# Kernel tuning notes

Hardware: AMD Instinct MI355X
Metric: run time of the kernel (lower is better)

## Reference

```python
import jax, jax.numpy as jnp
import numpy as np


def setup_inputs() -> dict:
    key = jax.random.key(0)
    k1, k2 = jax.random.split(key)
    B, C, H, W = 16, 32, 256, 256
    OH, OW = 256, 256
    Im = jax.random.normal(k1, (B, C, H, W), dtype=jnp.float32)
    # pixel-space sampling coordinates in [0, W-1] / [0, H-1]
    gx = jax.random.uniform(k2, (B, 1, OH, OW), dtype=jnp.float32) * (W - 1)
    gy = jax.random.uniform(jax.random.fold_in(k2, 1), (B, 1, OH, OW), dtype=jnp.float32) * (H - 1)
    G = jnp.concatenate([gx, gy], axis=1)  # [B, 2, OH, OW]
    return {"Im": Im, "G": G}


def reference(Im, G):
    # replicate-pad by 1 on each spatial side
    Imp = jnp.pad(Im, ((0, 0), (0, 0), (1, 1), (1, 1)), mode='edge')
    B, C, H, W = Imp.shape
    _, _, OH, OW = G.shape
    # flatten coords per batch; +1 accounts for the pad
    x = G[:, 0].reshape(B, -1) + 1.0  # [B, OH*OW]
    y = G[:, 1].reshape(B, -1) + 1.0
    max_x, max_y = W - 1, H - 1
    x0 = jnp.floor(x).astype(jnp.int32)
    y0 = jnp.floor(y).astype(jnp.int32)
    x1 = x0 + 1
    y1 = y0 + 1
    x0 = jnp.clip(x0, 0, max_x)
    x1 = jnp.clip(x1, 0, max_x)
    y0 = jnp.clip(y0, 0, max_y)
    y1 = jnp.clip(y1, 0, max_y)
    # [B, H*W, C] channels-last flat image, gather per batch
    Im_flat = Imp.transpose(0, 2, 3, 1).reshape(B, H * W, C)

    def gather(yi, xi):
        idx = yi * W + xi  # [B, OH*OW]
        return jnp.take_along_axis(Im_flat, idx[:, :, None], axis=1)  # [B, OH*OW, C]

    Ia = gather(y0, x0)
    Ib = gather(y1, x0)
    Ic = gather(y0, x1)
    Id = gather(y1, x1)
    dx = x1.astype(jnp.float32) - x  # note: uses clamped x1, as in the original
    dy = y1.astype(jnp.float32) - y
    wa = (dy * dx)[:, :, None]
    wb = ((1.0 - dy) * dx)[:, :, None]
    wc = (dy * (1.0 - dx))[:, :, None]
    wd = ((1.0 - dy) * (1.0 - dx))[:, :, None]
    out = wa * Ia + wb * Ib + wc * Ic + wd * Id  # [B, OH*OW, C]
    return out.reshape(B, OH, OW, C).transpose(0, 3, 1, 2)
```

## Files before the change

### kernel.cpp

```cpp
#include <hip/hip_runtime.h>

#define BB 16
#define CC 32
#define HH 256
#define WW 256
#define OHH 256
#define OWW 256
#define HW  (HH * WW)

typedef _Float16 half8 __attribute__((ext_vector_type(8)));
typedef _Float16 half4v __attribute__((ext_vector_type(4)));
typedef float float4v __attribute__((ext_vector_type(4)));

__global__ __launch_bounds__(256) void nchw_to_nhwc_h(
    const float* __restrict__ Im,
    _Float16* __restrict__ dst)
{
    __shared__ float lds[64 * 33];
    int blk  = blockIdx.x;
    int xcd  = blk & 7;
    int slot = blk >> 3;
    int b    = xcd + 8 * (slot >> 10);
    int inner = slot & 1023;
    int h  = inner >> 2;
    int w0 = (inner & 3) * 64;
    int t  = threadIdx.x;

    const float* src = Im + ((size_t)b * CC * HH + h) * WW;

    #pragma unroll
    for (int i = 0; i < 2; ++i) {
        int idx = i * 256 + t;
        int c  = idx >> 4;
        int wq = (idx & 15) * 4;
        float4v v = __builtin_nontemporal_load(
            (const float4v*)(src + (size_t)c * HW + w0 + wq));
        lds[(wq + 0) * 33 + c] = v.x;
        lds[(wq + 1) * 33 + c] = v.y;
        lds[(wq + 2) * 33 + c] = v.z;
        lds[(wq + 3) * 33 + c] = v.w;
    }
    __syncthreads();

    _Float16* dstp = dst + (((size_t)b * HH + h) * WW + w0) * CC;
    #pragma unroll
    for (int i = 0; i < 2; ++i) {
        int idx = i * 256 + t;
        int w  = idx >> 3;
        int c4 = (idx & 7) * 4;
        half4v v;
        v.x = (_Float16)lds[w * 33 + c4 + 0];
        v.y = (_Float16)lds[w * 33 + c4 + 1];
        v.z = (_Float16)lds[w * 33 + c4 + 2];
        v.w = (_Float16)lds[w * 33 + c4 + 3];
        *(half4v*)(dstp + w * CC + c4) = v;
    }
}

__global__ __launch_bounds__(256) void bilerp_gather_h(
    const _Float16* __restrict__ img,
    const float* __restrict__ G,
    float* __restrict__ out)
{
    int blk  = blockIdx.x;
    int xcd  = blk & 7;
    int slot = blk >> 3;
    int b    = xcd + 8 * (1 - (slot >> 9));
    int inner = slot & 511;
    int t    = threadIdx.x;
    int hid  = t & 1;
    int pixb = inner * 128 + (t >> 1);
    int ox = pixb & (OWW - 1);
    int oy = pixb >> 8;

    const float* Gb = G + (size_t)b * 2 * HW + oy * OWW + ox;
    float gx = __builtin_nontemporal_load(Gb);
    float gy = __builtin_nontemporal_load(Gb + HW);

    float x = gx + 1.0f;
    float y = gy + 1.0f;
    int x0 = (int)floorf(x);
    int y0 = (int)floorf(y);
    int x1 = x0 + 1;
    int y1 = y0 + 1;
    x0 = min(max(x0, 0), WW + 1);
    x1 = min(max(x1, 0), WW + 1);
    y0 = min(max(y0, 0), HH + 1);
    y1 = min(max(y1, 0), HH + 1);
    float dx = (float)x1 - x;
    float dy = (float)y1 - y;

    int xi0 = min(max(x0 - 1, 0), WW - 1);
    int xi1 = min(max(x1 - 1, 0), WW - 1);
    int yi0 = min(max(y0 - 1, 0), HH - 1);
    int yi1 = min(max(y1 - 1, 0), HH - 1);

    float wa = dy * dx;
    float wb = (1.0f - dy) * dx;
    float wc = dy * (1.0f - dx);
    float wd = (1.0f - dy) * (1.0f - dx);

    const _Float16* base = img + (size_t)b * HW * CC + hid * 16;
    const half8* pa = (const half8*)(base + ((size_t)yi0 * WW + xi0) * CC);
    const half8* pb = (const half8*)(base + ((size_t)yi1 * WW + xi0) * CC);
    const half8* pc = (const half8*)(base + ((size_t)yi0 * WW + xi1) * CC);
    const half8* pd = (const half8*)(base + ((size_t)yi1 * WW + xi1) * CC);

    half8 a0 = pa[0], a1 = pa[1];
    half8 b0 = pb[0], b1 = pb[1];
    half8 c0 = pc[0], c1 = pc[1];
    half8 d0 = pd[0], d1 = pd[1];

    float r[16];
    #pragma unroll
    for (int j = 0; j < 8; ++j) {
        r[j]     = wa * (float)a0[j] + wb * (float)b0[j]
                 + wc * (float)c0[j] + wd * (float)d0[j];
        r[j + 8] = wa * (float)a1[j] + wb * (float)b1[j]
                 + wc * (float)c1[j] + wd * (float)d1[j];
    }

    float* outp = out + ((size_t)b * CC + hid * 16) * HW + oy * OWW + ox;
    #pragma unroll
    for (int j = 0; j < 16; ++j) {
        __builtin_nontemporal_store(r[j], outp + j * HW);
    }
}

__global__ __launch_bounds__(256) void bilerp_direct(
    const float* __restrict__ Im, const float* __restrict__ G,
    float* __restrict__ out)
{
    int idx = blockIdx.x * blockDim.x + threadIdx.x;
    int ox = idx & (OWW - 1);
    int oy = (idx >> 8) & (OHH - 1);
    int b  = idx >> 16;

    const float* Gb = G + (size_t)b * 2 * HW + oy * OWW + ox;
    float x = Gb[0] + 1.0f;
    float y = Gb[HW] + 1.0f;
    int x0 = (int)floorf(x), y0 = (int)floorf(y);
    int x1 = x0 + 1, y1 = y0 + 1;
    x0 = min(max(x0, 0), WW + 1); x1 = min(max(x1, 0), WW + 1);
    y0 = min(max(y0, 0), HH + 1); y1 = min(max(y1, 0), HH + 1);
    float dx = (float)x1 - x, dy = (float)y1 - y;
    int xi0 = min(max(x0 - 1, 0), WW - 1), xi1 = min(max(x1 - 1, 0), WW - 1);
    int yi0 = min(max(y0 - 1, 0), HH - 1), yi1 = min(max(y1 - 1, 0), HH - 1);
    float wa = dy * dx, wb = (1.0f - dy) * dx;
    float wc = dy * (1.0f - dx), wd = (1.0f - dy) * (1.0f - dx);

    const float* Ibase = Im + (size_t)b * CC * HW;
    int o00 = yi0 * WW + xi0, o01 = yi0 * WW + xi1;
    int o10 = yi1 * WW + xi0, o11 = yi1 * WW + xi1;
    float* outp = out + (size_t)b * CC * HW + oy * OWW + ox;
    #pragma unroll 4
    for (int c = 0; c < CC; ++c) {
        const float* p = Ibase + c * HW;
        outp[c * HW] = wa * p[o00] + wb * p[o10] + wc * p[o01] + wd * p[o11];
    }
}

extern "C" void kernel_launch(void* const* d_in, const int* in_sizes, int n_in,
                              void* d_out, int out_size, void* d_ws, size_t ws_size,
                              hipStream_t stream) {
    const float* Im = (const float*)d_in[0];
    const float* G  = (const float*)d_in[1];
    float* out = (float*)d_out;

    const size_t needed = (size_t)BB * HW * CC * sizeof(_Float16);
    int total = BB * OHH * OWW;

    if (ws_size >= needed) {
        _Float16* nhwc = (_Float16*)d_ws;
        nchw_to_nhwc_h<<<dim3(BB * HH * (WW / 64)), dim3(256), 0, stream>>>(Im, nhwc);
        bilerp_gather_h<<<dim3(2 * total / 256), dim3(256), 0, stream>>>(nhwc, G, out);
    } else {
        bilerp_direct<<<dim3(total / 256), dim3(256), 0, stream>>>(Im, G, out);
    }
}
```

Before: 267.1 us.

## Overlap half the transpose with half the gather in a mixed kernel

Splits the work into three launches. The first transposes batches 8-15 to NHWC fp16. A mixed kernel then gathers for batches 8-15 while interleaved blocks transpose batches 0-7, and a final pass gathers batches 0-7. The transpose store is also widened to half8, with nontemporal stores for the tiles written in the mixed pass. The aim is to overlap the bandwidth-bound transpose with the latency-bound gather and keep the transposed data hot in cache, at the cost of an extra launch and mixed block types.

```diff
diff --git a/kernel.cpp b/kernel.cpp
--- a/kernel.cpp
+++ b/kernel.cpp
@@ -8,26 +8,19 @@
 #define OWW 256
 #define HW  (HH * WW)
 
+#define TBLK_HALF (8 * HH * (WW / 64))
+#define GBLK_HALF (8 * (HW / 128))
+#define MIX_BLOCKS (TBLK_HALF + GBLK_HALF)
+
 typedef _Float16 half8 __attribute__((ext_vector_type(8)));
-typedef _Float16 half4v __attribute__((ext_vector_type(4)));
 typedef float float4v __attribute__((ext_vector_type(4)));
 
-__global__ __launch_bounds__(256) void nchw_to_nhwc_h(
-    const float* __restrict__ Im,
-    _Float16* __restrict__ dst)
+__device__ __forceinline__ void transpose_tile(
+    const float* __restrict__ Im, _Float16* __restrict__ img,
+    int b, int h, int w0, bool nt, float* lds)
 {
-    __shared__ float lds[64 * 33];
-    int blk  = blockIdx.x;
-    int xcd  = blk & 7;
-    int slot = blk >> 3;
-    int b    = xcd + 8 * (slot >> 10);
-    int inner = slot & 1023;
-    int h  = inner >> 2;
-    int w0 = (inner & 3) * 64;
-    int t  = threadIdx.x;
-
+    int t = threadIdx.x;
     const float* src = Im + ((size_t)b * CC * HH + h) * WW;
-
     #pragma unroll
     for (int i = 0; i < 2; ++i) {
         int idx = i * 256 + t;
@@ -41,39 +34,26 @@
         lds[(wq + 3) * 33 + c] = v.w;
     }
     __syncthreads();
-
-    _Float16* dstp = dst + (((size_t)b * HH + h) * WW + w0) * CC;
+    int w  = t >> 2;
+    int c8 = (t & 3) * 8;
+    half8 v;
     #pragma unroll
-    for (int i = 0; i < 2; ++i) {
-        int idx = i * 256 + t;
-        int w  = idx >> 3;
-        int c4 = (idx & 7) * 4;
-        half4v v;
-        v.x = (_Float16)lds[w * 33 + c4 + 0];
-        v.y = (_Float16)lds[w * 33 + c4 + 1];
-        v.z = (_Float16)lds[w * 33 + c4 + 2];
-        v.w = (_Float16)lds[w * 33 + c4 + 3];
-        *(half4v*)(dstp + w * CC + c4) = v;
-    }
+    for (int j = 0; j < 8; ++j)
+        v[j] = (_Float16)lds[w * 33 + c8 + j];
+    _Float16* dstp = img + (((size_t)b * HH + h) * WW + w0 + w) * CC + c8;
+    if (nt) __builtin_nontemporal_store(v, (half8*)dstp);
+    else    *(half8*)dstp = v;
 }
 
-__global__ __launch_bounds__(256) void bilerp_gather_h(
-    const _Float16* __restrict__ img,
-    const float* __restrict__ G,
-    float* __restrict__ out)
+__device__ __forceinline__ void gather_unit(
+    const _Float16* __restrict__ img, const float* __restrict__ G,
+    float* __restrict__ out, int b, int u)
 {
-    int blk  = blockIdx.x;
-    int xcd  = blk & 7;
-    int slot = blk >> 3;
-    int b    = xcd + 8 * (1 - (slot >> 9));
-    int inner = slot & 511;
     int t    = threadIdx.x;
     int hid  = t & 1;
-    int pixb = inner * 128 + (t >> 1);
-    int ox = pixb & (OWW - 1);
-    int oy = pixb >> 8;
+    int pixb = u * 128 + (t >> 1);
 
-    const float* Gb = G + (size_t)b * 2 * HW + oy * OWW + ox;
+    const float* Gb = G + (size_t)b * 2 * HW + pixb;
     float gx = __builtin_nontemporal_load(Gb);
     float gy = __builtin_nontemporal_load(Gb + HW);
 
@@ -120,11 +100,46 @@
                  + wc * (float)c1[j] + wd * (float)d1[j];
     }
 
-    float* outp = out + ((size_t)b * CC + hid * 16) * HW + oy * OWW + ox;
+    float* outp = out + ((size_t)b * CC + hid * 16) * HW + pixb;
     #pragma unroll
     for (int j = 0; j < 16; ++j) {
         __builtin_nontemporal_store(r[j], outp + j * HW);
     }
+}
+
+__global__ __launch_bounds__(256) void tpass1(
+    const float* __restrict__ Im, _Float16* __restrict__ img)
+{
+    __shared__ float lds[64 * 33];
+    int m = blockIdx.x;
+    int b = 8 + (m & 7);
+    int slot = m >> 3;
+    transpose_tile(Im, img, b, slot >> 2, (slot & 3) * 64, false, lds);
+}
+
+__global__ __launch_bounds__(256) void mixpass(
+    const float* __restrict__ Im, _Float16* __restrict__ img,
+    const float* __restrict__ G, float* __restrict__ out)
+{
+    __shared__ float lds[64 * 33];
+    int m = blockIdx.x;
+    int q = m / 24;
+    int r = m - q * 24;
+    if (r < 8) {
+        gather_unit(img, G, out, 8 + r, q);
+    } else {
+        int xcd = r & 7;
+        int ti  = q * 2 + (r >> 4);
+        transpose_tile(Im, img, xcd, ti >> 2, (ti & 3) * 64, true, lds);
+    }
+}
+
+__global__ __launch_bounds__(256) void gpass3(
+    const _Float16* __restrict__ img, const float* __restrict__ G,
+    float* __restrict__ out)
+{
+    int m = blockIdx.x;
+    gather_unit(img, G, out, m & 7, m >> 3);
 }
 
 __global__ __launch_bounds__(256) void bilerp_direct(
@@ -172,8 +187,9 @@
 
     if (ws_size >= needed) {
         _Float16* nhwc = (_Float16*)d_ws;
-        nchw_to_nhwc_h<<<dim3(BB * HH * (WW / 64)), dim3(256), 0, stream>>>(Im, nhwc);
-        bilerp_gather_h<<<dim3(2 * total / 256), dim3(256), 0, stream>>>(nhwc, G, out);
+        tpass1 <<<dim3(TBLK_HALF),  dim3(256), 0, stream>>>(Im, nhwc);
+        mixpass<<<dim3(MIX_BLOCKS), dim3(256), 0, stream>>>(Im, nhwc, G, out);
+        gpass3 <<<dim3(GBLK_HALF),  dim3(256), 0, stream>>>(nhwc, G, out);
     } else {
         bilerp_direct<<<dim3(total / 256), dim3(256), 0, stream>>>(Im, G, out);
     }
```

Measured after the change: 263.8 us, median of 2. About the same (-1.2%).
